# Kernel tuning notes

Measured on AMD Instinct MI355X. Metric: run time of the kernel, lower is better.

The kernel has to match this reference:

```python
import jax, jax.numpy as jnp
import numpy as np

C = 64
G = 4
K = 3
GC = C // G
OS = 1.0  # offset_scale
OM_DIM = int(np.ceil(G * K * K * 3 / 8) * 8)  # 112, padded; only first G*27 used


def setup_inputs() -> dict:
    key = jax.random.key(0)
    ks = jax.random.split(key, 8)
    B, H, W = 2, 384, 384
    s = 0.02
    return {
        "inp": jax.random.normal(ks[0], (B, C, H, W), jnp.float32),
        "Wv": jax.random.normal(ks[1], (C, C), jnp.float32) * s,
        "bv": jnp.zeros((C,), jnp.float32),
        "Wdw": jax.random.normal(ks[2], (C, 1, K, K), jnp.float32) * s,
        "bdw": jnp.zeros((C,), jnp.float32),
        "Wom": jax.random.normal(ks[3], (C, OM_DIM), jnp.float32) * s,
        "bom": jnp.zeros((OM_DIM,), jnp.float32),
        "Wo": jax.random.normal(ks[4], (C, C), jnp.float32) * s,
    }


def _bilinear(v, px, py, H, W, b_idx, g_idx):
    # v: (B,H,W,G,GC); px,py: (B,H,W,G) pixel coords; zero padding outside.
    x0 = jnp.floor(px)
    y0 = jnp.floor(py)
    wx1 = px - x0
    wy1 = py - y0
    x0i = x0.astype(jnp.int32)
    y0i = y0.astype(jnp.int32)
    out = jnp.zeros(px.shape + (v.shape[-1],), v.dtype)
    for dy, wy in ((0, 1.0 - wy1), (1, wy1)):
        for dx, wx in ((0, 1.0 - wx1), (1, wx1)):
            xi = x0i + dx
            yi = y0i + dy
            valid = ((xi >= 0) & (xi < W) & (yi >= 0) & (yi < H)).astype(v.dtype)
            xc = jnp.clip(xi, 0, W - 1)
            yc = jnp.clip(yi, 0, H - 1)
            g = v[b_idx, yc, xc, g_idx]  # (B,H,W,G,GC)
            out = out + g * (wy * wx * valid)[..., None]
    return out


def reference(inp, Wv, bv, Wdw, bdw, Wom, bom, Wo):
    B, _, H, W = inp.shape
    x = inp.transpose(0, 2, 3, 1)  # (B,H,W,C)
    # value projection, split into groups
    value = (x @ Wv + bv).reshape(B, H, W, G, GC)
    # depthwise conv on input feeds the offset/mask predictor
    dw = jax.lax.conv_general_dilated(
        inp, Wdw, window_strides=(1, 1), padding=[(1, 1), (1, 1)],
        feature_group_count=C) + bdw[None, :, None, None]
    om = dw.transpose(0, 2, 3, 1) @ Wom + bom  # (B,H,W,OM_DIM)
    om = om[..., : G * K * K * 3].reshape(B, H, W, G, K * K * 3)
    off = om[..., : K * K * 2].reshape(B, H, W, G, K * K, 2)  # (dx,dy) per point
    mask = om[..., K * K * 2:]  # (B,H,W,G,K*K), no softmax in DCNv4

    base_x = jnp.arange(W, dtype=value.dtype)[None, None, :, None]
    base_y = jnp.arange(H, dtype=value.dtype)[None, :, None, None]
    b_idx = jnp.arange(B)[:, None, None, None]
    g_idx = jnp.arange(G)[None, None, None, :]

    out = jnp.zeros((B, H, W, G, GC), value.dtype)
    k = 0
    for ky in range(K):
        for kx in range(K):
            dx = off[..., k, 0]
            dy = off[..., k, 1]
            px = base_x + ((kx - K // 2) + dx) * OS
            py = base_y + ((ky - K // 2) + dy) * OS
            samp = _bilinear(value, px, py, H, W, b_idx, g_idx)
            out = out + samp * mask[..., k][..., None]
            k += 1

    out = out.reshape(B, H, W, C) @ Wo  # output_proj, no bias (output_bias=False)
    return out.transpose(0, 3, 1, 2)  # back to (B,C,H,W)
```

## Files before the change

### kernel.cpp

```cpp
#include <hip/hip_runtime.h>
#include <hip/hip_fp16.h>
#include <math.h>

namespace {
constexpr int kH = 384, kW = 384, kBn = 2;
constexpr int kHW = kH * kW;
constexpr int kOMD = 112;
constexpr int kNB = kBn * (kHW / 64);
constexpr int kNB8 = kNB / 8;
}

typedef _Float16 h2 __attribute__((ext_vector_type(2)));

__device__ unsigned g_Wom2[32 * kOMD];
__device__ unsigned g_Wo2[32 * 64];

__device__ __forceinline__ int swz(int t) {
    return (t & 7) * kNB8 + (t >> 3);
}

__device__ __forceinline__ unsigned pack2h(float a, float b) {
    unsigned short lo = __builtin_bit_cast(unsigned short, __float2half_rn(a));
    unsigned short hi = __builtin_bit_cast(unsigned short, __float2half_rn(b));
    return (unsigned)lo | ((unsigned)hi << 16);
}

#if __has_builtin(__builtin_amdgcn_fdot2)
__device__ __forceinline__ float dot2(unsigned a, unsigned b, float c) {
    return __builtin_amdgcn_fdot2(__builtin_bit_cast(h2, a),
                                  __builtin_bit_cast(h2, b), c, false);
}
#else
__device__ __forceinline__ float dot2(unsigned a, unsigned b, float c) {
    h2 ha = __builtin_bit_cast(h2, a), hb = __builtin_bit_cast(h2, b);
    c = fmaf((float)ha.x, (float)hb.x, c);
    c = fmaf((float)ha.y, (float)hb.y, c);
    return c;
}
#endif

__device__ __forceinline__ void fma2h(float& a0, float& a1, float w, unsigned u) {
    __half2 h = __builtin_bit_cast(__half2, u);
    a0 = fmaf(w, __half2float(h.x), a0);
    a1 = fmaf(w, __half2float(h.y), a1);
}

__global__ __launch_bounds__(256) void k_value(
        const float* __restrict__ inp, const float* __restrict__ Wv,
        const float* __restrict__ bv, const float* __restrict__ Wom,
        const float* __restrict__ Wo, unsigned short* __restrict__ value) {
    __shared__ float xin[64][64];
    const int tid = threadIdx.x;

    if (blockIdx.x == 0) {
        for (int i = tid; i < 32 * kOMD; i += 256) {
            const int ci2 = i / kOMD, j = i % kOMD;
            g_Wom2[i] = pack2h(Wom[(2 * ci2) * kOMD + j],
                               Wom[(2 * ci2 + 1) * kOMD + j]);
        }
        for (int i = tid; i < 32 * 64; i += 256) {
            const int ci2 = i >> 6, j = i & 63;
            g_Wo2[i] = pack2h(Wo[(2 * ci2) * 64 + j],
                              Wo[(2 * ci2 + 1) * 64 + j]);
        }
    }

    const int bid = swz(blockIdx.x);
    const int b = bid / (kHW / 64);
    const int pix0 = (bid % (kHW / 64)) * 64;
    const float* ib = inp + (size_t)b * 64 * kHW + pix0;
    for (int i = tid; i < 1024; i += 256) {
        const int c = i >> 4, p4 = (i & 15) << 2;
        const float4 v = *(const float4*)(ib + (size_t)c * kHW + p4);
        *(float4*)&xin[c][p4] = v;
    }
    __syncthreads();

    const int p = tid & 63;
    const int gs = __builtin_amdgcn_readfirstlane(tid >> 6);

    float acc[16];
    {
        const float* bg = bv + gs * 16;
        #pragma unroll
        for (int j = 0; j < 16; ++j) acc[j] = bg[j];
    }
    #pragma unroll 4
    for (int ci = 0; ci < 64; ++ci) {
        const float a = xin[ci][p];
        const float* wr = Wv + ci * 64 + gs * 16;
        #pragma unroll
        for (int j = 0; j < 16; ++j) acc[j] = fmaf(a, wr[j], acc[j]);
    }

    unsigned u[8];
    #pragma unroll
    for (int j = 0; j < 8; ++j) u[j] = pack2h(acc[2 * j], acc[2 * j + 1]);
    uint4* vo = (uint4*)(value + ((size_t)(b * 4 + gs) * kHW + pix0 + p) * 16);
    vo[0] = make_uint4(u[0], u[1], u[2], u[3]);
    vo[1] = make_uint4(u[4], u[5], u[6], u[7]);
}

__global__ __launch_bounds__(256) void k_main(
        const float* __restrict__ inp, const float* __restrict__ Wdw,
        const float* __restrict__ bdw, const float* __restrict__ bom,
        const unsigned short* __restrict__ value, float* __restrict__ out) {
    __shared__ unsigned lds2[32][64];

    const int tid = threadIdx.x;
    const int bid = swz(blockIdx.x);
    const int b = bid / (kH * (kW / 64));
    const int rem = bid % (kH * (kW / 64));
    const int h = rem / (kW / 64);
    const int w0 = (rem % (kW / 64)) * 64;

    const int p = tid & 63;
    const int gs = __builtin_amdgcn_readfirstlane(tid >> 6);

    {
        const int w = w0 + p;
        #pragma unroll 2
        for (int q = 0; q < 8; ++q) {
            float sv[2];
            #pragma unroll
            for (int e = 0; e < 2; ++e) {
                const int c = gs * 16 + 2 * q + e;
                const float* ib = inp + (size_t)(b * 64 + c) * kHW;
                float s = bdw[c];
                #pragma unroll
                for (int r = 0; r < 3; ++r) {
                    const int y = h - 1 + r;
                    if (y >= 0 && y < kH) {
                        const float* rowp = ib + (size_t)y * kW;
                        #pragma unroll
                        for (int kx = 0; kx < 3; ++kx) {
                            const int x = w - 1 + kx;
                            const float v = (x >= 0 && x < kW) ? rowp[x] : 0.f;
                            s = fmaf(v, Wdw[c * 9 + r * 3 + kx], s);
                        }
                    }
                }
                sv[e] = s;
            }
            lds2[gs * 8 + q][p] = pack2h(sv[0], sv[1]);
        }
    }
    __syncthreads();

    float om[27];
    {
        const float* bg = bom + gs * 27;
        #pragma unroll
        for (int j = 0; j < 27; ++j) om[j] = bg[j];
        #pragma unroll 4
        for (int ci2 = 0; ci2 < 32; ++ci2) {
            const unsigned a2 = lds2[ci2][p];
            const unsigned* wr = g_Wom2 + ci2 * kOMD + gs * 27;
            #pragma unroll
            for (int j = 0; j < 27; ++j) om[j] = dot2(a2, wr[j], om[j]);
        }
    }
    __syncthreads();

    {
        float acc[16];
        #pragma unroll
        for (int j = 0; j < 16; ++j) acc[j] = 0.f;
        const float fw = (float)(w0 + p);
        const float fh = (float)h;
        const unsigned short* vbase = value + (size_t)(b * 4 + gs) * kHW * 16;
        #pragma unroll
        for (int k = 0; k < 9; ++k) {
            const int ky = k / 3, kx = k % 3;
            const float dx = om[2 * k];
            const float dy = om[2 * k + 1];
            const float m = om[18 + k];
            const float px = fw + (float)(kx - 1) + dx;
            const float py = fh + (float)(ky - 1) + dy;
            const float x0f = floorf(px), y0f = floorf(py);
            const int x0 = (int)x0f, y0 = (int)y0f;
            const float wx1 = px - x0f, wy1 = py - y0f;
            const float wx0 = 1.f - wx1, wy0 = 1.f - wy1;
            #pragma unroll
            for (int cor = 0; cor < 4; ++cor) {
                const int dy2 = cor >> 1, dx2 = cor & 1;
                const int xi = x0 + dx2, yi = y0 + dy2;
                float wgt = (dy2 ? wy1 : wy0) * (dx2 ? wx1 : wx0) * m;
                if (xi < 0 || xi >= kW || yi < 0 || yi >= kH) wgt = 0.f;
                const int xc = min(max(xi, 0), kW - 1);
                const int yc = min(max(yi, 0), kH - 1);
                const uint4* vp = (const uint4*)(vbase +
                        ((size_t)yc * kW + xc) * 16);
                const uint4 u0 = vp[0];
                const uint4 u1 = vp[1];
                fma2h(acc[0],  acc[1],  wgt, u0.x);
                fma2h(acc[2],  acc[3],  wgt, u0.y);
                fma2h(acc[4],  acc[5],  wgt, u0.z);
                fma2h(acc[6],  acc[7],  wgt, u0.w);
                fma2h(acc[8],  acc[9],  wgt, u1.x);
                fma2h(acc[10], acc[11], wgt, u1.y);
                fma2h(acc[12], acc[13], wgt, u1.z);
                fma2h(acc[14], acc[15], wgt, u1.w);
            }
        }
        #pragma unroll
        for (int j = 0; j < 8; ++j)
            lds2[gs * 8 + j][p] = pack2h(acc[2 * j], acc[2 * j + 1]);
    }
    __syncthreads();

    {
        float acc[16];
        #pragma unroll
        for (int j = 0; j < 16; ++j) acc[j] = 0.f;
        #pragma unroll 4
        for (int ci2 = 0; ci2 < 32; ++ci2) {
            const unsigned a2 = lds2[ci2][p];
            const unsigned* wr = g_Wo2 + ci2 * 64 + gs * 16;
            #pragma unroll
            for (int j = 0; j < 16; ++j) acc[j] = dot2(a2, wr[j], acc[j]);
        }
        float* ob = out + (size_t)(b * 64 + gs * 16) * kHW + (size_t)h * kW + w0 + p;
        #pragma unroll
        for (int j = 0; j < 16; ++j) ob[(size_t)j * kHW] = acc[j];
    }
}

extern "C" void kernel_launch(void* const* d_in, const int* in_sizes, int n_in,
                              void* d_out, int out_size, void* d_ws, size_t ws_size,
                              hipStream_t stream) {
    const float* inp = (const float*)d_in[0];
    const float* Wv  = (const float*)d_in[1];
    const float* bv  = (const float*)d_in[2];
    const float* Wdw = (const float*)d_in[3];
    const float* bdw = (const float*)d_in[4];
    const float* Wom = (const float*)d_in[5];
    const float* bom = (const float*)d_in[6];
    const float* Wo  = (const float*)d_in[7];
    float* outp = (float*)d_out;
    unsigned short* value = (unsigned short*)d_ws;

    k_value<<<kNB, 256, 0, stream>>>(inp, Wv, bv, Wom, Wo, value);
    k_main<<<kNB, 256, 0, stream>>>(inp, Wdw, bdw, bom, value, outp);
}
```

Baseline: 304.8 us.

## Use MFMA 16x16x32 f16 for offset/mask and output projections

Replaces the per-thread fdot2 loops for the offset/mask projection and the output projection with MFMA 16x16x32 f16 matrix instructions. Weights are pre-swizzled into fragment layout in global memory, and activations are staged in LDS in the B-fragment layout. Offset/mask results go through an LDS transpose buffer stored as f16, so om values lose some precision compared with the earlier f32 accumulation. The LDS layout and synchronisation between stages change to fit this scheme.

```diff
diff --git a/kernel.cpp b/kernel.cpp
--- a/kernel.cpp
+++ b/kernel.cpp
@@ -10,10 +10,11 @@
 constexpr int kNB8 = kNB / 8;
 }
 
-typedef _Float16 h2 __attribute__((ext_vector_type(2)));
-
-__device__ unsigned g_Wom2[32 * kOMD];
-__device__ unsigned g_Wo2[32 * 64];
+typedef _Float16 half8 __attribute__((ext_vector_type(8)));
+typedef float f32x4 __attribute__((ext_vector_type(4)));
+
+__device__ __align__(16) _Float16 g_WomF[8 * 2 * 64 * 8];
+__device__ __align__(16) _Float16 g_WoF[4 * 2 * 64 * 8];
 
 __device__ __forceinline__ int swz(int t) {
     return (t & 7) * kNB8 + (t >> 3);
@@ -25,24 +26,23 @@
     return (unsigned)lo | ((unsigned)hi << 16);
 }
 
-#if __has_builtin(__builtin_amdgcn_fdot2)
-__device__ __forceinline__ float dot2(unsigned a, unsigned b, float c) {
-    return __builtin_amdgcn_fdot2(__builtin_bit_cast(h2, a),
-                                  __builtin_bit_cast(h2, b), c, false);
-}
-#else
-__device__ __forceinline__ float dot2(unsigned a, unsigned b, float c) {
-    h2 ha = __builtin_bit_cast(h2, a), hb = __builtin_bit_cast(h2, b);
-    c = fmaf((float)ha.x, (float)hb.x, c);
-    c = fmaf((float)ha.y, (float)hb.y, c);
-    return c;
-}
-#endif
+__device__ __forceinline__ float h2f_lo(unsigned u) {
+    __half2 h = __builtin_bit_cast(__half2, u);
+    return __half2float(h.x);
+}
+__device__ __forceinline__ float h2f_hi(unsigned u) {
+    __half2 h = __builtin_bit_cast(__half2, u);
+    return __half2float(h.y);
+}
 
 __device__ __forceinline__ void fma2h(float& a0, float& a1, float w, unsigned u) {
     __half2 h = __builtin_bit_cast(__half2, u);
     a0 = fmaf(w, __half2float(h.x), a0);
     a1 = fmaf(w, __half2float(h.y), a1);
+}
+
+__device__ __forceinline__ half8 ld_frag_g(const _Float16* ptr) {
+    return __builtin_bit_cast(half8, *(const uint4*)ptr);
 }
 
 __global__ __launch_bounds__(256) void k_value(
@@ -53,15 +53,19 @@
     const int tid = threadIdx.x;
 
     if (blockIdx.x == 0) {
-        for (int i = tid; i < 32 * kOMD; i += 256) {
-            const int ci2 = i / kOMD, j = i % kOMD;
-            g_Wom2[i] = pack2h(Wom[(2 * ci2) * kOMD + j],
-                               Wom[(2 * ci2 + 1) * kOMD + j]);
-        }
-        for (int i = tid; i < 32 * 64; i += 256) {
-            const int ci2 = i >> 6, j = i & 63;
-            g_Wo2[i] = pack2h(Wo[(2 * ci2) * 64 + j],
-                              Wo[(2 * ci2 + 1) * 64 + j]);
+        for (int i = tid; i < 8 * 2 * 64 * 8; i += 256) {
+            const int jj = i & 7, l = (i >> 3) & 63, kh = (i >> 9) & 1, jt = i >> 10;
+            const int slot = jt * 16 + (l & 15);
+            const int g = slot >> 5, j = slot & 31;
+            const int ch = kh * 32 + ((l >> 4) & 3) * 8 + jj;
+            const float v = (j < 27) ? Wom[ch * kOMD + g * 27 + j] : 0.f;
+            g_WomF[i] = (_Float16)v;
+        }
+        for (int i = tid; i < 4 * 2 * 64 * 8; i += 256) {
+            const int jj = i & 7, l = (i >> 3) & 63, kh = (i >> 9) & 1, mt = i >> 10;
+            const int co = mt * 16 + (l & 15);
+            const int ch = kh * 32 + ((l >> 4) & 3) * 8 + jj;
+            g_WoF[i] = (_Float16)Wo[ch * 64 + co];
         }
     }
 
@@ -105,7 +109,8 @@
         const float* __restrict__ inp, const float* __restrict__ Wdw,
         const float* __restrict__ bdw, const float* __restrict__ bom,
         const unsigned short* __restrict__ value, float* __restrict__ out) {
-    __shared__ unsigned lds2[32][64];
+    __shared__ unsigned bact[8][64][4];
+    __shared__ unsigned short omlh[64][136];
 
     const int tid = threadIdx.x;
     const int bid = swz(blockIdx.x);
@@ -115,54 +120,80 @@
     const int w0 = (rem % (kW / 64)) * 64;
 
     const int p = tid & 63;
+    const int q = p >> 4, lr = p & 15;
     const int gs = __builtin_amdgcn_readfirstlane(tid >> 6);
 
     {
         const int w = w0 + p;
-        #pragma unroll 2
-        for (int q = 0; q < 8; ++q) {
-            float sv[2];
+        float sv[16];
+        #pragma unroll 4
+        for (int cc = 0; cc < 16; ++cc) {
+            const int c = gs * 16 + cc;
+            const float* ib = inp + (size_t)(b * 64 + c) * kHW;
+            float s = bdw[c];
             #pragma unroll
-            for (int e = 0; e < 2; ++e) {
-                const int c = gs * 16 + 2 * q + e;
-                const float* ib = inp + (size_t)(b * 64 + c) * kHW;
-                float s = bdw[c];
-                #pragma unroll
-                for (int r = 0; r < 3; ++r) {
-                    const int y = h - 1 + r;
-                    if (y >= 0 && y < kH) {
-                        const float* rowp = ib + (size_t)y * kW;
-                        #pragma unroll
-                        for (int kx = 0; kx < 3; ++kx) {
-                            const int x = w - 1 + kx;
-                            const float v = (x >= 0 && x < kW) ? rowp[x] : 0.f;
-                            s = fmaf(v, Wdw[c * 9 + r * 3 + kx], s);
-                        }
+            for (int r = 0; r < 3; ++r) {
+                const int y = h - 1 + r;
+                if (y >= 0 && y < kH) {
+                    const float* rowp = ib + (size_t)y * kW;
+                    #pragma unroll
+                    for (int kx = 0; kx < 3; ++kx) {
+                        const int x = w - 1 + kx;
+                        const float v = (x >= 0 && x < kW) ? rowp[x] : 0.f;
+                        s = fmaf(v, Wdw[c * 9 + r * 3 + kx], s);
                     }
                 }
-                sv[e] = s;
             }
-            lds2[gs * 8 + q][p] = pack2h(sv[0], sv[1]);
-        }
-    }
-    __syncthreads();
-
-    float om[27];
-    {
-        const float* bg = bom + gs * 27;
-        #pragma unroll
-        for (int j = 0; j < 27; ++j) om[j] = bg[j];
-        #pragma unroll 4
-        for (int ci2 = 0; ci2 < 32; ++ci2) {
-            const unsigned a2 = lds2[ci2][p];
-            const unsigned* wr = g_Wom2 + ci2 * kOMD + gs * 27;
+            sv[cc] = s;
+        }
+        unsigned u[8];
+        #pragma unroll
+        for (int j = 0; j < 8; ++j) u[j] = pack2h(sv[2 * j], sv[2 * j + 1]);
+        *(uint4*)&bact[2 * gs][p][0]     = make_uint4(u[0], u[1], u[2], u[3]);
+        *(uint4*)&bact[2 * gs + 1][p][0] = make_uint4(u[4], u[5], u[6], u[7]);
+    }
+    __syncthreads();
+
+    {
+        half8 bfr[2];
+        #pragma unroll
+        for (int kh = 0; kh < 2; ++kh)
+            bfr[kh] = __builtin_bit_cast(half8,
+                    *(const uint4*)&bact[kh * 4 + q][gs * 16 + lr][0]);
+        const int px = gs * 16 + lr;
+        #pragma unroll
+        for (int jt = 0; jt < 8; ++jt) {
+            const half8 a0 = ld_frag_g(g_WomF + ((jt * 2 + 0) * 64 + p) * 8);
+            const half8 a1 = ld_frag_g(g_WomF + ((jt * 2 + 1) * 64 + p) * 8);
+            f32x4 acc = {0.f, 0.f, 0.f, 0.f};
+            acc = __builtin_amdgcn_mfma_f32_16x16x32_f16(a0, bfr[0], acc, 0, 0, 0);
+            acc = __builtin_amdgcn_mfma_f32_16x16x32_f16(a1, bfr[1], acc, 0, 0, 0);
+            uint2 st;
+            st.x = pack2h(acc[0], acc[1]);
+            st.y = pack2h(acc[2], acc[3]);
+            *(uint2*)&omlh[px][jt * 16 + q * 4] = st;
+        }
+    }
+    __syncthreads();
+
+    {
+        float om[27];
+        {
+            const unsigned short* orow = &omlh[p][gs * 32];
+            const uint4 r0 = *(const uint4*)(orow);
+            const uint4 r1 = *(const uint4*)(orow + 8);
+            const uint4 r2 = *(const uint4*)(orow + 16);
+            const uint2 r3 = *(const uint2*)(orow + 24);
+            const unsigned rr[14] = {r0.x, r0.y, r0.z, r0.w, r1.x, r1.y, r1.z, r1.w,
+                                     r2.x, r2.y, r2.z, r2.w, r3.x, r3.y};
+            const float* bg = bom + gs * 27;
             #pragma unroll
-            for (int j = 0; j < 27; ++j) om[j] = dot2(a2, wr[j], om[j]);
-        }
-    }
-    __syncthreads();
-
-    {
+            for (int j = 0; j < 27; ++j) {
+                const float v = (j & 1) ? h2f_hi(rr[j >> 1]) : h2f_lo(rr[j >> 1]);
+                om[j] = bg[j] + v;
+            }
+        }
+
         float acc[16];
         #pragma unroll
         for (int j = 0; j < 16; ++j) acc[j] = 0.f;
@@ -203,26 +234,35 @@
                 fma2h(acc[14], acc[15], wgt, u1.w);
             }
         }
-        #pragma unroll
-        for (int j = 0; j < 8; ++j)
-            lds2[gs * 8 + j][p] = pack2h(acc[2 * j], acc[2 * j + 1]);
-    }
-    __syncthreads();
-
-    {
-        float acc[16];
-        #pragma unroll
-        for (int j = 0; j < 16; ++j) acc[j] = 0.f;
-        #pragma unroll 4
-        for (int ci2 = 0; ci2 < 32; ++ci2) {
-            const unsigned a2 = lds2[ci2][p];
-            const unsigned* wr = g_Wo2 + ci2 * 64 + gs * 16;
-            #pragma unroll
-            for (int j = 0; j < 16; ++j) acc[j] = dot2(a2, wr[j], acc[j]);
-        }
-        float* ob = out + (size_t)(b * 64 + gs * 16) * kHW + (size_t)h * kW + w0 + p;
-        #pragma unroll
-        for (int j = 0; j < 16; ++j) ob[(size_t)j * kHW] = acc[j];
+        unsigned u[8];
+        #pragma unroll
+        for (int j = 0; j < 8; ++j) u[j] = pack2h(acc[2 * j], acc[2 * j + 1]);
+        *(uint4*)&bact[2 * gs][p][0]     = make_uint4(u[0], u[1], u[2], u[3]);
+        *(uint4*)&bact[2 * gs + 1][p][0] = make_uint4(u[4], u[5], u[6], u[7]);
+    }
+    __syncthreads();
+
+    {
+        half8 sfr[2];
+        #pragma unroll
+        for (int kh = 0; kh < 2; ++kh)
+            sfr[kh] = __builtin_bit_cast(half8,
+                    *(const uint4*)&bact[kh * 4 + q][gs * 16 + lr][0]);
+        const int px = gs * 16 + lr;
+        #pragma unroll
+        for (int mt = 0; mt < 4; ++mt) {
+            const half8 a0 = ld_frag_g(g_WoF + ((mt * 2 + 0) * 64 + p) * 8);
+            const half8 a1 = ld_frag_g(g_WoF + ((mt * 2 + 1) * 64 + p) * 8);
+            f32x4 acc = {0.f, 0.f, 0.f, 0.f};
+            acc = __builtin_amdgcn_mfma_f32_16x16x32_f16(a0, sfr[0], acc, 0, 0, 0);
+            acc = __builtin_amdgcn_mfma_f32_16x16x32_f16(a1, sfr[1], acc, 0, 0, 0);
+            float* ob = out + (size_t)(b * 64 + mt * 16 + q * 4) * kHW
+                            + (size_t)h * kW + w0 + px;
+            ob[0]            = acc[0];
+            ob[kHW]          = acc[1];
+            ob[2 * (size_t)kHW] = acc[2];
+            ob[3 * (size_t)kHW] = acc[3];
+        }
     }
 }
 
```

After: 350.9 us. 1.15x slower.
